# Kernel optimization log

Measured on AMD Instinct MI355X. Metric: run time of the kernel, lower is better.

Reference implementation:

```python
import jax, jax.numpy as jnp
import numpy as np

N = 8192        # num nodes
E = 262144      # edges per relation (avg degree 32)
R = 2           # number of edge relations in edge_index_dict
F = 111         # num_feature
D = 32          # embedding_dim
H = 256         # hidden_dim
C = 15          # num_classes (pooled cluster count)


def setup_inputs() -> dict:
    key = jax.random.key(0)
    ks = jax.random.split(key, 9)
    x_note = jax.random.normal(ks[0], (N, F), dtype=jnp.float32)
    edges = jax.random.randint(ks[1], (R, 2, E), 0, N, dtype=jnp.int32)
    s = 0.1
    W_embed = jax.random.normal(ks[2], (F, D), dtype=jnp.float32) * s
    b_embed = jnp.zeros((D,), jnp.float32)
    W_self = jax.random.normal(ks[3], (R, D, H), dtype=jnp.float32) * s
    W_neigh = jax.random.normal(ks[4], (R, D, H), dtype=jnp.float32) * s
    b_gnn = jnp.zeros((R, H), jnp.float32)
    W_s1 = jax.random.normal(ks[5], (H, C), dtype=jnp.float32) * s
    W_s2 = jax.random.normal(ks[6], (H, C), dtype=jnp.float32) * s
    return dict(x_note=x_note, edges=edges, W_embed=W_embed, b_embed=b_embed,
                W_self=W_self, W_neigh=W_neigh, b_gnn=b_gnn, W_s1=W_s1, W_s2=W_s2)


def _coord_to_adj(edges, n):
    # edges: [R, 2, E] -> dense adjacency [R, n, n] via a single scatter per relation
    def one(e):
        return jnp.zeros((n, n), jnp.float32).at[e[0], e[1]].set(1.0)
    return jax.vmap(one)(edges)


def _hetero_gnn(x, edges, W_self, W_neigh, b, n):
    # per-relation SAGEConv (mean aggregation), summed over relations, ReLU
    def one(e, ws, wn, bb):
        src, dst = e[0], e[1]
        msg_sum = jax.ops.segment_sum(x[src], dst, num_segments=n)      # [n, D]
        cnt = jax.ops.segment_sum(jnp.ones((e.shape[1],), x.dtype), dst, num_segments=n)
        mean = msg_sum / jnp.maximum(cnt, 1.0)[:, None]
        return x @ ws + mean @ wn + bb
    outs = jax.vmap(one)(edges, W_self, W_neigh, b)  # [R, n, H]
    return jax.nn.relu(outs.sum(0))


def _gnn_cluster(x, adj, W_s):
    # DiffPool-style: S = softmax(A_sum X W_s); X' = S^T X; A'_r = S^T A_r S
    a_sum = adj.sum(0)                                  # [n, n]
    S = jax.nn.softmax((a_sum @ x) @ W_s, axis=-1)      # [n, C]
    x_p = S.T @ x                                       # [C, H]
    tmp = jnp.einsum('rnm,mc->rnc', adj, S)             # [R, n, C]
    adj_p = jnp.einsum('nk,rnc->rkc', S, tmp)           # [R, C, C]
    return x_p, adj_p, S


def reference(x_note, edges, W_embed, b_embed, W_self, W_neigh, b_gnn, W_s1, W_s2):
    n = x_note.shape[0]
    x = x_note @ W_embed + b_embed                      # linear_embed
    adj = _coord_to_adj(edges, n)                       # coord_to_adj
    x = _hetero_gnn(x, edges, W_self, W_neigh, b_gnn, n)  # gnn_embed
    x, adj, S1 = _gnn_cluster(x, adj, W_s1)             # gnn_cluster1
    x, adj, S2 = _gnn_cluster(x, adj, W_s2)             # gnn_cluster2
    return (x, S1, S2)
```

## Files before the change

kernel.cpp:

```cpp
#include <hip/hip_runtime.h>
#include <hip/hip_bf16.h>

#define N_NODES 8192
#define E_EDGES 262144
#define R_REL   2
#define F_FEAT  111
#define D_EMB   32
#define H_HID   256
#define C_CLS   15
#define DCAP2   96
#define SCAP    96
#define BMW     256


__global__ void k_prep(const float* __restrict__ x_note, const float* __restrict__ W,
                       const float* __restrict__ b, float* __restrict__ X0,
                       const int* __restrict__ edges, int* __restrict__ deg,
                       int* __restrict__ colD2,
                       const float* __restrict__ Wself, const float* __restrict__ Wneigh,
                       float* __restrict__ W96) {
    int blk = blockIdx.x;
    if (blk < 1024) {
        __shared__ float Ws[F_FEAT * D_EMB];
        for (int i = threadIdx.x; i < F_FEAT * D_EMB; i += blockDim.x) Ws[i] = W[i];
        __syncthreads();
        int tid = blk * 256 + threadIdx.x;
        int n = tid >> 5, d = tid & 31;
        const float* xr = x_note + n * F_FEAT;
        float acc = b[d];
        for (int f = 0; f < F_FEAT; ++f) acc += xr[f] * Ws[f * D_EMB + d];
        X0[n * D_EMB + d] = acc;
    } else if (blk < 3072) {
        int i = (blk - 1024) * 256 + threadIdx.x;
        int r = i >> 18, e = i & (E_EDGES - 1);
        int src = edges[(r * 2) * E_EDGES + e];
        int dst = edges[(r * 2 + 1) * E_EDGES + e];
        int pos = atomicAdd(&deg[(2 + r) * N_NODES + dst], 1);
        if (pos < DCAP2) colD2[(r * N_NODES + dst) * DCAP2 + pos] = src;
    } else {
        int i = (blk - 3072) * 256 + threadIdx.x;
        int dd = i >> 8, h = i & 255;
        float v;
        if (dd < 32)      v = Wself[dd * 256 + h] + Wself[(32 + dd) * 256 + h];
        else if (dd < 64) v = Wneigh[(dd - 32) * 256 + h];
        else              v = Wneigh[(32 + dd - 64) * 256 + h];
        W96[i] = v;
    }
}

__global__ __launch_bounds__(256) void k_dedup_mean(const int* __restrict__ deg,
                                                    const int* __restrict__ colD2,
                                                    int* __restrict__ degS,
                                                    int* __restrict__ colS2,
                                                    const float* __restrict__ X0,
                                                    float* __restrict__ xin) {
    __shared__ int buf[4][DCAP2];
    __shared__ unsigned int bm[4][BMW];
    int w = threadIdx.x >> 6, lane = threadIdx.x & 63;
    int row = blockIdx.x * 4 + w;
    int r = row >> 13, n = row & (N_NODES - 1);
    int lenRaw = deg[(2 + r) * N_NODES + n];
    int lim = (lenRaw < DCAP2) ? lenRaw : DCAP2;
    const int* base = colD2 + (r * N_NODES + n) * DCAP2;
    #pragma unroll
    for (int q = 0; q < BMW / 64; ++q) bm[w][lane + q * 64] = 0u;
    for (int i = lane; i < lim; i += 64) buf[w][i] = base[i];
    __syncthreads();
    for (int i = lane; i < lim; i += 64) {
        int v = buf[w][i];
        unsigned int bit = 1u << (v & 31);
        unsigned int old = atomicOr(&bm[w][v >> 5], bit);
        if (!(old & bit)) {
            int pos = atomicAdd(&degS[r * N_NODES + v], 1);
            if (pos < SCAP) colS2[(r * N_NODES + v) * SCAP + pos] = n;
        }
    }
    int d = lane & 31, h = lane >> 5;
    float a0 = 0.f, a1 = 0.f, a2 = 0.f, a3 = 0.f;
    int i = h;
    for (; i + 6 < lim; i += 8) {
        int c0 = buf[w][i], c1 = buf[w][i + 2], c2 = buf[w][i + 4], c3 = buf[w][i + 6];
        a0 += X0[c0 * D_EMB + d]; a1 += X0[c1 * D_EMB + d];
        a2 += X0[c2 * D_EMB + d]; a3 += X0[c3 * D_EMB + d];
    }
    for (; i < lim; i += 2) a0 += X0[buf[w][i] * D_EMB + d];
    float acc = ((a0 + a1) + (a2 + a3));
    acc += __shfl_down(acc, 32, 64);
    if (lane < 32) {
        float inv = 1.f / fmaxf((float)lenRaw, 1.f);
        xin[n * 96 + 32 + r * 32 + d] = acc * inv;
        if (r == 0) xin[n * 96 + d] = X0[n * D_EMB + d];
    }
}

__global__ __launch_bounds__(256) void k_gemm_g1(const float* __restrict__ xin,
                                                 const float* __restrict__ W96,
                                                 const float* __restrict__ bg,
                                                 const float* __restrict__ Ws1,
                                                 float* __restrict__ H1,
                                                 float* __restrict__ G1) {
    __shared__ float As[64][97];
    __shared__ float Bs[96][64];
    int g = blockIdx.x;
    int bm = g >> 2, bn = g & 3;
    int t = threadIdx.x;
    int nb = bm * 64, cb = bn * 64;
    for (int i = t; i < 64 * 96; i += 256) { int row = i / 96, k = i - row * 96; As[row][k] = xin[(nb + row) * 96 + k]; }
    for (int i = t; i < 96 * 64; i += 256) { int k = i >> 6, col = i & 63; Bs[k][col] = W96[k * 256 + cb + col]; }
    __syncthreads();
    int tx = t & 15, ty = t >> 4;
    float acc[4][4] = {};
    #pragma unroll 4
    for (int k = 0; k < 96; ++k) {
        float a0 = As[ty * 4 + 0][k], a1 = As[ty * 4 + 1][k], a2 = As[ty * 4 + 2][k], a3 = As[ty * 4 + 3][k];
        float b0 = Bs[k][tx * 4 + 0], b1 = Bs[k][tx * 4 + 1], b2 = Bs[k][tx * 4 + 2], b3 = Bs[k][tx * 4 + 3];
        acc[0][0] += a0 * b0; acc[0][1] += a0 * b1; acc[0][2] += a0 * b2; acc[0][3] += a0 * b3;
        acc[1][0] += a1 * b0; acc[1][1] += a1 * b1; acc[1][2] += a1 * b2; acc[1][3] += a1 * b3;
        acc[2][0] += a2 * b0; acc[2][1] += a2 * b1; acc[2][2] += a2 * b2; acc[2][3] += a2 * b3;
        acc[3][0] += a3 * b0; acc[3][1] += a3 * b1; acc[3][2] += a3 * b2; acc[3][3] += a3 * b3;
    }
    float hv[4][4];
    #pragma unroll
    for (int i = 0; i < 4; ++i) {
        int n = nb + ty * 4 + i;
        #pragma unroll
        for (int j = 0; j < 4; ++j) {
            int c = cb + tx * 4 + j;
            hv[i][j] = fmaxf(acc[i][j] + bg[c] + bg[H_HID + c], 0.f);
            H1[n * H_HID + c] = hv[i][j];
        }
    }
    __syncthreads();
    float* Wg = &Bs[0][0];
    #pragma unroll
    for (int i = 0; i < 4; ++i)
        #pragma unroll
        for (int j = 0; j < 4; ++j)
            As[ty * 4 + i][tx * 4 + j] = hv[i][j];
    for (int idx = t; idx < 64 * C_CLS; idx += 256) {
        int j = idx / C_CLS, c = idx - j * C_CLS;
        Wg[j * 16 + c] = Ws1[(cb + j) * C_CLS + c];
    }
    __syncthreads();
    for (int task = t; task < 64 * C_CLS; task += 256) {
        int row = task / C_CLS, c = task - row * C_CLS;
        float s = 0.f;
        #pragma unroll 8
        for (int j = 0; j < 64; ++j) s += As[row][j] * Wg[j * 16 + c];
        atomicAdd(&G1[(nb + row) * 16 + c], s);
    }
}

__global__ __launch_bounds__(256) void k_logits_sm(const int* __restrict__ deg,
                                                   const int* __restrict__ colS2,
                                                   const float* __restrict__ G1,
                                                   float* __restrict__ S1,
                                                   float* __restrict__ S1p) {
    int n = (blockIdx.x * blockDim.x + threadIdx.x) >> 4;
    int c = threadIdx.x & 15;
    float a0 = 0.f, a1 = 0.f, a2 = 0.f, a3 = 0.f, a4 = 0.f, a5 = 0.f, a6 = 0.f, a7 = 0.f;
    for (int r = 0; r < R_REL; ++r) {
        int len = deg[r * N_NODES + n];
        if (len > SCAP) len = SCAP;
        const int* cr = colS2 + (r * N_NODES + n) * SCAP;
        int idx = 0;
        for (; idx + 8 <= len; idx += 8) {
            int c0 = cr[idx + 0], c1 = cr[idx + 1], c2 = cr[idx + 2], c3 = cr[idx + 3];
            int c4 = cr[idx + 4], c5 = cr[idx + 5], c6 = cr[idx + 6], c7 = cr[idx + 7];
            a0 += G1[c0 * 16 + c]; a1 += G1[c1 * 16 + c];
            a2 += G1[c2 * 16 + c]; a3 += G1[c3 * 16 + c];
            a4 += G1[c4 * 16 + c]; a5 += G1[c5 * 16 + c];
            a6 += G1[c6 * 16 + c]; a7 += G1[c7 * 16 + c];
        }
        for (; idx < len; ++idx) a0 += G1[cr[idx] * 16 + c];
    }
    float logit = (c < C_CLS) ? (((a0 + a1) + (a2 + a3)) + ((a4 + a5) + (a6 + a7))) : -1e30f;
    float m = logit;
    for (int off = 8; off; off >>= 1) m = fmaxf(m, __shfl_xor(m, off, 16));
    float e = (c < C_CLS) ? expf(logit - m) : 0.f;
    float ssum = e;
    for (int off = 8; off; off >>= 1) ssum += __shfl_xor(ssum, off, 16);
    float p = e / ssum;
    if (c < C_CLS) S1[n * C_CLS + c] = p;
    S1p[n * 16 + c] = (c < C_CLS) ? p : 0.f;
}

__global__ __launch_bounds__(256) void k_xpT(const float* __restrict__ S1p, const float* __restrict__ H1,
                                             float* __restrict__ xp,
                                             const int* __restrict__ deg, const int* __restrict__ colS2,
                                             float* __restrict__ partial) {
    __shared__ float Tl[16][16];
    int blk = blockIdx.x;
    if (blk < 128) {
        int h = threadIdx.x;
        int base = blk * 64;
        float acc[C_CLS];
        #pragma unroll
        for (int c = 0; c < C_CLS; ++c) acc[c] = 0.f;
        for (int i = 0; i < 64; ++i) {
            int n = base + i;
            float hv = H1[n * H_HID + h];
            const float* sr = S1p + n * 16;
            #pragma unroll
            for (int c = 0; c < C_CLS; ++c) acc[c] += sr[c] * hv;
        }
        #pragma unroll
        for (int c = 0; c < C_CLS; ++c) atomicAdd(&xp[c * H_HID + h], acc[c]);
    } else {
        int bb = blk - 128;
        int g = threadIdx.x >> 4, c = threadIdx.x & 15;
        int n0 = bb * 16;
        int n = n0 + g;
        float a0 = 0.f, a1 = 0.f, a2 = 0.f, a3 = 0.f, a4 = 0.f, a5 = 0.f, a6 = 0.f, a7 = 0.f;
        for (int r = 0; r < R_REL; ++r) {
            int len = deg[r * N_NODES + n];
            if (len > SCAP) len = SCAP;
            const int* cr = colS2 + (r * N_NODES + n) * SCAP;
            int idx = 0;
            for (; idx + 8 <= len; idx += 8) {
                int c0 = cr[idx + 0], c1 = cr[idx + 1], c2 = cr[idx + 2], c3 = cr[idx + 3];
                int c4 = cr[idx + 4], c5 = cr[idx + 5], c6 = cr[idx + 6], c7 = cr[idx + 7];
                a0 += S1p[c0 * 16 + c]; a1 += S1p[c1 * 16 + c];
                a2 += S1p[c2 * 16 + c]; a3 += S1p[c3 * 16 + c];
                a4 += S1p[c4 * 16 + c]; a5 += S1p[c5 * 16 + c];
                a6 += S1p[c6 * 16 + c]; a7 += S1p[c7 * 16 + c];
            }
            for (; idx < len; ++idx) a0 += S1p[cr[idx] * 16 + c];
        }
        float tval = ((a0 + a1) + (a2 + a3)) + ((a4 + a5) + (a6 + a7));
        Tl[g][c] = (c < C_CLS) ? tval : 0.f;
        __syncthreads();
        int t = threadIdx.x;
        if (t < C_CLS * C_CLS) {
            int k = t / C_CLS, cc = t - k * C_CLS;
            float s = 0.f;
            #pragma unroll
            for (int i = 0; i < 16; ++i) s += S1p[(n0 + i) * 16 + k] * Tl[i][cc];
            partial[bb * (C_CLS * C_CLS) + t] = s;
        }
    }
}

__global__ void k_cluster2(const float* __restrict__ partialAdj, const float* __restrict__ xp,
                           const float* __restrict__ Ws2, float* __restrict__ out_x,
                           float* __restrict__ out_S2) {
    __shared__ float a2[C_CLS * C_CLS];
    __shared__ float xps[C_CLS * H_HID];
    __shared__ float y2[C_CLS * H_HID];
    __shared__ float lg[C_CLS * C_CLS];
    __shared__ float S2s[C_CLS * C_CLS];
    int t = threadIdx.x;
    if (t < C_CLS * C_CLS) {
        float s0 = 0.f, s1 = 0.f, s2 = 0.f, s3 = 0.f;
        for (int b = 0; b < 512; b += 4) {
            s0 += partialAdj[(b + 0) * (C_CLS * C_CLS) + t];
            s1 += partialAdj[(b + 1) * (C_CLS * C_CLS) + t];
            s2 += partialAdj[(b + 2) * (C_CLS * C_CLS) + t];
            s3 += partialAdj[(b + 3) * (C_CLS * C_CLS) + t];
        }
        a2[t] = (s0 + s1) + (s2 + s3);
    }
    for (int i = t; i < C_CLS * H_HID; i += 256) xps[i] = xp[i];
    __syncthreads();
    for (int i = 0; i < C_CLS; ++i) {
        float acc = 0.f;
        #pragma unroll
        for (int j = 0; j < C_CLS; ++j) acc += a2[i * C_CLS + j] * xps[j * H_HID + t];
        y2[i * H_HID + t] = acc;
    }
    __syncthreads();
    for (int idx = t; idx < C_CLS * C_CLS; idx += 256) {
        int i = idx / C_CLS, c = idx % C_CLS;
        float acc = 0.f;
        for (int h = 0; h < H_HID; ++h) acc += y2[i * H_HID + h] * Ws2[h * C_CLS + c];
        lg[idx] = acc;
    }
    __syncthreads();
    if (t < C_CLS) {
        float m = -1e30f;
        for (int c = 0; c < C_CLS; ++c) m = fmaxf(m, lg[t * C_CLS + c]);
        float s = 0.f;
        for (int c = 0; c < C_CLS; ++c) { float ev = expf(lg[t * C_CLS + c] - m); S2s[t * C_CLS + c] = ev; s += ev; }
        for (int c = 0; c < C_CLS; ++c) { S2s[t * C_CLS + c] /= s; out_S2[t * C_CLS + c] = S2s[t * C_CLS + c]; }
    }
    __syncthreads();
    for (int c = 0; c < C_CLS; ++c) {
        float acc = 0.f;
        #pragma unroll
        for (int i = 0; i < C_CLS; ++i) acc += S2s[i * C_CLS + c] * xps[i * H_HID + t];
        out_x[c * H_HID + t] = acc;
    }
}

extern "C" void kernel_launch(void* const* d_in, const int* in_sizes, int n_in,
                              void* d_out, int out_size, void* d_ws, size_t ws_size,
                              hipStream_t stream) {
    const float* x_note  = (const float*)d_in[0];
    const int*   edges   = (const int*)d_in[1];
    const float* W_embed = (const float*)d_in[2];
    const float* b_embed = (const float*)d_in[3];
    const float* W_self  = (const float*)d_in[4];
    const float* W_neigh = (const float*)d_in[5];
    const float* b_gnn   = (const float*)d_in[6];
    const float* W_s1    = (const float*)d_in[7];
    const float* W_s2    = (const float*)d_in[8];
    float* out = (float*)d_out;

    float* out_x  = out;
    float* out_S1 = out + C_CLS * H_HID;
    float* out_S2 = out + C_CLS * H_HID + N_NODES * C_CLS;

    char* ws = (char*)d_ws;
    size_t off = 0;
    auto alloc = [&](size_t bytes) { size_t p = off; off += (bytes + 255) & ~(size_t)255; return p; };
    size_t regionA = alloc((size_t)18 * 1024 * 1024);
    size_t oDeg    = alloc((size_t)4 * N_NODES * 4);
    size_t oXp     = alloc((size_t)C_CLS * H_HID * 4);
    size_t oG1     = alloc((size_t)N_NODES * 16 * 4);
    size_t zeroEnd = off;
    size_t oX0     = alloc((size_t)N_NODES * D_EMB * 4);
    size_t oPart   = alloc((size_t)512 * C_CLS * C_CLS * 4);
    size_t oW96    = alloc((size_t)96 * H_HID * 4);

    int*   colD2  = (int*)(ws + regionA);
    float* H1     = (float*)(ws + regionA);
    int*   colS2  = (int*)(ws + regionA + (size_t)8 * 1024 * 1024);
    float* S1p    = (float*)(ws + regionA + (size_t)14 * 1024 * 1024);
    float* xin    = (float*)(ws + regionA + (size_t)14 * 1024 * 1024 + 512 * 1024);
    int*   deg    = (int*)(ws + oDeg);
    float* xp     = (float*)(ws + oXp);
    float* G1     = (float*)(ws + oG1);
    float* X0     = (float*)(ws + oX0);
    float* partialAdj = (float*)(ws + oPart);
    float* W96    = (float*)(ws + oW96);

    hipMemsetAsync(ws + oDeg, 0, zeroEnd - oDeg, stream);

    k_prep<<<3168, 256, 0, stream>>>(x_note, W_embed, b_embed, X0, edges, deg, colD2,
                                     W_self, W_neigh, W96);
    k_dedup_mean<<<4096, 256, 0, stream>>>(deg, colD2, deg, colS2, X0, xin);
    k_gemm_g1<<<512, 256, 0, stream>>>(xin, W96, b_gnn, W_s1, H1, G1);
    k_logits_sm<<<(N_NODES * 16) / 256, 256, 0, stream>>>(deg, colS2, G1, out_S1, S1p);
    k_xpT<<<128 + 512, 256, 0, stream>>>(S1p, H1, xp, deg, colS2, partialAdj);
    k_cluster2<<<1, 256, 0, stream>>>(partialAdj, xp, W_s2, out_x, out_S2);
}
```

Measured before the change: 135.5 us.

## Double thread parallelism per row in dedup, logits and adjacency gather kernels

Assigns 128 threads per adjacency row in the dedup/mean kernel instead of 64, combining the halves through shared memory. The logits and S^T A S gather kernels now split the two relations across two 16-lane groups and merge them with a shuffle. k_xpT moves to 512-thread blocks with half as many xp blocks. The aim is more memory-level parallelism on the latency-bound irregular gathers, at the cost of more blocks, an extra barrier and some idle lanes when rows have low degree.

```diff
diff --git a/kernel.cpp b/kernel.cpp
--- a/kernel.cpp
+++ b/kernel.cpp
@@ -54,22 +54,23 @@
                                                     int* __restrict__ colS2,
                                                     const float* __restrict__ X0,
                                                     float* __restrict__ xin) {
-    __shared__ int buf[4][DCAP2];
-    __shared__ unsigned int bm[4][BMW];
-    int w = threadIdx.x >> 6, lane = threadIdx.x & 63;
-    int row = blockIdx.x * 4 + w;
+    __shared__ int buf[2][DCAP2];
+    __shared__ unsigned int bm[2][BMW];
+    __shared__ float red[2][D_EMB];
+    int w2 = threadIdx.x >> 7;
+    int lane = threadIdx.x & 127;
+    int row = blockIdx.x * 2 + w2;
     int r = row >> 13, n = row & (N_NODES - 1);
     int lenRaw = deg[(2 + r) * N_NODES + n];
     int lim = (lenRaw < DCAP2) ? lenRaw : DCAP2;
     const int* base = colD2 + (r * N_NODES + n) * DCAP2;
-    #pragma unroll
-    for (int q = 0; q < BMW / 64; ++q) bm[w][lane + q * 64] = 0u;
-    for (int i = lane; i < lim; i += 64) buf[w][i] = base[i];
-    __syncthreads();
-    for (int i = lane; i < lim; i += 64) {
-        int v = buf[w][i];
+    bm[w2][lane] = 0u; bm[w2][lane + 128] = 0u;
+    if (lane < lim) buf[w2][lane] = base[lane];
+    __syncthreads();
+    if (lane < lim) {
+        int v = buf[w2][lane];
         unsigned int bit = 1u << (v & 31);
-        unsigned int old = atomicOr(&bm[w][v >> 5], bit);
+        unsigned int old = atomicOr(&bm[w2][v >> 5], bit);
         if (!(old & bit)) {
             int pos = atomicAdd(&degS[r * N_NODES + v], 1);
             if (pos < SCAP) colS2[(r * N_NODES + v) * SCAP + pos] = n;
@@ -78,17 +79,20 @@
     int d = lane & 31, h = lane >> 5;
     float a0 = 0.f, a1 = 0.f, a2 = 0.f, a3 = 0.f;
     int i = h;
-    for (; i + 6 < lim; i += 8) {
-        int c0 = buf[w][i], c1 = buf[w][i + 2], c2 = buf[w][i + 4], c3 = buf[w][i + 6];
+    for (; i + 12 < lim; i += 16) {
+        int c0 = buf[w2][i], c1 = buf[w2][i + 4], c2 = buf[w2][i + 8], c3 = buf[w2][i + 12];
         a0 += X0[c0 * D_EMB + d]; a1 += X0[c1 * D_EMB + d];
         a2 += X0[c2 * D_EMB + d]; a3 += X0[c3 * D_EMB + d];
     }
-    for (; i < lim; i += 2) a0 += X0[buf[w][i] * D_EMB + d];
+    for (; i < lim; i += 4) a0 += X0[buf[w2][i] * D_EMB + d];
     float acc = ((a0 + a1) + (a2 + a3));
     acc += __shfl_down(acc, 32, 64);
+    if (lane >= 64 && lane < 96) red[w2][d] = acc;
+    __syncthreads();
     if (lane < 32) {
+        float total = acc + red[w2][d];
         float inv = 1.f / fmaxf((float)lenRaw, 1.f);
-        xin[n * 96 + 32 + r * 32 + d] = acc * inv;
+        xin[n * 96 + 32 + r * 32 + d] = total * inv;
         if (r == 0) xin[n * 96 + d] = X0[n * D_EMB + d];
     }
 }
@@ -156,13 +160,14 @@
                                                    const float* __restrict__ G1,
                                                    float* __restrict__ S1,
                                                    float* __restrict__ S1p) {
-    int n = (blockIdx.x * blockDim.x + threadIdx.x) >> 4;
+    int n = (blockIdx.x * 256 + threadIdx.x) >> 5;
+    int sub = (threadIdx.x >> 4) & 1;
     int c = threadIdx.x & 15;
     float a0 = 0.f, a1 = 0.f, a2 = 0.f, a3 = 0.f, a4 = 0.f, a5 = 0.f, a6 = 0.f, a7 = 0.f;
-    for (int r = 0; r < R_REL; ++r) {
-        int len = deg[r * N_NODES + n];
+    {
+        int len = deg[sub * N_NODES + n];
         if (len > SCAP) len = SCAP;
-        const int* cr = colS2 + (r * N_NODES + n) * SCAP;
+        const int* cr = colS2 + (sub * N_NODES + n) * SCAP;
         int idx = 0;
         for (; idx + 8 <= len; idx += 8) {
             int c0 = cr[idx + 0], c1 = cr[idx + 1], c2 = cr[idx + 2], c3 = cr[idx + 3];
@@ -174,26 +179,30 @@
         }
         for (; idx < len; ++idx) a0 += G1[cr[idx] * 16 + c];
     }
-    float logit = (c < C_CLS) ? (((a0 + a1) + (a2 + a3)) + ((a4 + a5) + (a6 + a7))) : -1e30f;
+    float part = (((a0 + a1) + (a2 + a3)) + ((a4 + a5) + (a6 + a7)));
+    float sum = part + __shfl_xor(part, 16, 32);
+    float logit = (c < C_CLS) ? sum : -1e30f;
     float m = logit;
     for (int off = 8; off; off >>= 1) m = fmaxf(m, __shfl_xor(m, off, 16));
     float e = (c < C_CLS) ? expf(logit - m) : 0.f;
     float ssum = e;
     for (int off = 8; off; off >>= 1) ssum += __shfl_xor(ssum, off, 16);
     float p = e / ssum;
-    if (c < C_CLS) S1[n * C_CLS + c] = p;
-    S1p[n * 16 + c] = (c < C_CLS) ? p : 0.f;
-}
-
-__global__ __launch_bounds__(256) void k_xpT(const float* __restrict__ S1p, const float* __restrict__ H1,
+    if (sub == 0) {
+        if (c < C_CLS) S1[n * C_CLS + c] = p;
+        S1p[n * 16 + c] = (c < C_CLS) ? p : 0.f;
+    }
+}
+
+__global__ __launch_bounds__(512) void k_xpT(const float* __restrict__ S1p, const float* __restrict__ H1,
                                              float* __restrict__ xp,
                                              const int* __restrict__ deg, const int* __restrict__ colS2,
                                              float* __restrict__ partial) {
     __shared__ float Tl[16][16];
     int blk = blockIdx.x;
-    if (blk < 128) {
-        int h = threadIdx.x;
-        int base = blk * 64;
+    if (blk < 64) {
+        int h = threadIdx.x & 255, seg = threadIdx.x >> 8;
+        int base = blk * 128 + seg * 64;
         float acc[C_CLS];
         #pragma unroll
         for (int c = 0; c < C_CLS; ++c) acc[c] = 0.f;
@@ -207,15 +216,17 @@
         #pragma unroll
         for (int c = 0; c < C_CLS; ++c) atomicAdd(&xp[c * H_HID + h], acc[c]);
     } else {
-        int bb = blk - 128;
-        int g = threadIdx.x >> 4, c = threadIdx.x & 15;
+        int bb = blk - 64;
+        int g = threadIdx.x >> 5;
+        int sub = (threadIdx.x >> 4) & 1;
+        int c = threadIdx.x & 15;
         int n0 = bb * 16;
         int n = n0 + g;
         float a0 = 0.f, a1 = 0.f, a2 = 0.f, a3 = 0.f, a4 = 0.f, a5 = 0.f, a6 = 0.f, a7 = 0.f;
-        for (int r = 0; r < R_REL; ++r) {
-            int len = deg[r * N_NODES + n];
+        {
+            int len = deg[sub * N_NODES + n];
             if (len > SCAP) len = SCAP;
-            const int* cr = colS2 + (r * N_NODES + n) * SCAP;
+            const int* cr = colS2 + (sub * N_NODES + n) * SCAP;
             int idx = 0;
             for (; idx + 8 <= len; idx += 8) {
                 int c0 = cr[idx + 0], c1 = cr[idx + 1], c2 = cr[idx + 2], c3 = cr[idx + 3];
@@ -227,8 +238,9 @@
             }
             for (; idx < len; ++idx) a0 += S1p[cr[idx] * 16 + c];
         }
-        float tval = ((a0 + a1) + (a2 + a3)) + ((a4 + a5) + (a6 + a7));
-        Tl[g][c] = (c < C_CLS) ? tval : 0.f;
+        float part = (((a0 + a1) + (a2 + a3)) + ((a4 + a5) + (a6 + a7)));
+        float tval = part + __shfl_xor(part, 16, 32);
+        if (sub == 0) Tl[g][c] = (c < C_CLS) ? tval : 0.f;
         __syncthreads();
         int t = threadIdx.x;
         if (t < C_CLS * C_CLS) {
@@ -338,9 +350,9 @@
 
     k_prep<<<3168, 256, 0, stream>>>(x_note, W_embed, b_embed, X0, edges, deg, colD2,
                                      W_self, W_neigh, W96);
-    k_dedup_mean<<<4096, 256, 0, stream>>>(deg, colD2, deg, colS2, X0, xin);
+    k_dedup_mean<<<8192, 256, 0, stream>>>(deg, colD2, deg, colS2, X0, xin);
     k_gemm_g1<<<512, 256, 0, stream>>>(xin, W96, b_gnn, W_s1, H1, G1);
-    k_logits_sm<<<(N_NODES * 16) / 256, 256, 0, stream>>>(deg, colS2, G1, out_S1, S1p);
-    k_xpT<<<128 + 512, 256, 0, stream>>>(S1p, H1, xp, deg, colS2, partialAdj);
+    k_logits_sm<<<1024, 256, 0, stream>>>(deg, colS2, G1, out_S1, S1p);
+    k_xpT<<<64 + 512, 512, 0, stream>>>(S1p, H1, xp, deg, colS2, partialAdj);
     k_cluster2<<<1, 256, 0, stream>>>(partialAdj, xp, W_s2, out_x, out_S2);
 }
```

After: 139.4 us. 2.9% more time.
